# Optimization experiments

Measured on AMD Instinct MI355X. Metric: run time of the kernel, lower is better.

Reference implementation:

```python
import jax, jax.numpy as jnp
import numpy as np

N_NODES = 100000

def sage_conv(x, edge_index, W_l, b_l, W_r):
    # PyG SAGEConv (aggr='mean'): out = lin_l(mean_{j in N(i)} x_j) + lin_r(x_i)
    src = edge_index[0]  # message source nodes
    dst = edge_index[1]  # aggregation target nodes
    msgs = x[src]                                   # [E, F] gather
    agg = jax.ops.segment_sum(msgs, dst, num_segments=N_NODES)      # [N, F]
    cnt = jax.ops.segment_sum(jnp.ones((edge_index.shape[1],), x.dtype), dst,
                              num_segments=N_NODES)                 # [N]
    mean = agg / jnp.clip(cnt, 1.0)[:, None]
    return mean @ W_l.T + b_l + x @ W_r.T


def setup_inputs() -> dict:
    key = jax.random.key(0)
    ks = jax.random.split(key, 8)
    num_features, hid, num_classes = 500, 8, 10
    n_edges = 3200000
    x = jax.random.normal(ks[0], (N_NODES, num_features), dtype=jnp.float32)
    edge_index = jax.random.randint(ks[1], (2, n_edges), 0, N_NODES, dtype=jnp.int64)
    def lin(k, fan_in, fan_out):
        bound = 1.0 / np.sqrt(fan_in)
        return jax.random.uniform(k, (fan_out, fan_in), jnp.float32, -bound, bound)
    W1_l = lin(ks[2], num_features, hid)
    b1_l = jax.random.uniform(ks[3], (hid,), jnp.float32, -1/np.sqrt(num_features), 1/np.sqrt(num_features))
    W1_r = lin(ks[4], num_features, hid)
    W2_l = lin(ks[5], hid, num_classes)
    b2_l = jax.random.uniform(ks[6], (num_classes,), jnp.float32, -1/np.sqrt(hid), 1/np.sqrt(hid))
    W2_r = lin(ks[7], hid, num_classes)
    return {"x": x, "edge_index": edge_index,
            "W1_l": W1_l, "b1_l": b1_l, "W1_r": W1_r,
            "W2_l": W2_l, "b2_l": b2_l, "W2_r": W2_r}


def reference(x, edge_index, W1_l, b1_l, W1_r, W2_l, b2_l, W2_r):
    # eval mode: dropout is a no-op
    h = sage_conv(x, edge_index, W1_l, b1_l, W1_r)
    h = jax.nn.elu(h)
    out = sage_conv(h, edge_index, W2_l, b2_l, W2_r)
    return jax.nn.log_softmax(out, axis=1)
```

## Files before the change

### kernel.cpp

```cpp
#include <hip/hip_runtime.h>
#include <hip/hip_bf16.h>
#include <math.h>


#define NBKT_MAX 1600
#define P_BLOCKS 256
#define BSH 6
#define BSZ 64
#define SEG_CAP 4096

typedef float f4v __attribute__((ext_vector_type(4)));

__device__ __forceinline__ float dot4(f4v a, f4v b) {
    return a.x * b.x + a.y * b.y + a.z * b.z + a.w * b.w;
}
__device__ __forceinline__ unsigned f2bf(float f) {
    unsigned u = __float_as_uint(f);
    return (u + 0x7FFFu + ((u >> 16) & 1u)) >> 16;
}
__device__ __forceinline__ float bflo(unsigned w) { return __uint_as_float(w << 16); }
__device__ __forceinline__ float bfhi(unsigned w) { return __uint_as_float(w & 0xFFFF0000u); }

__global__ __launch_bounds__(256) void proj1_kernel(
    const float* __restrict__ x,
    const float* __restrict__ W1l,
    const float* __restrict__ W1r,
    unsigned short* __restrict__ yab,
    float* __restrict__ yr,
    int N)
{
    const int lane = threadIdx.x & 63;
    const int wv   = threadIdx.x >> 6;
    const f4v zero = {0.f, 0.f, 0.f, 0.f};

    f4v wA[16], wB[16];
    #pragma unroll
    for (int m = 0; m < 16; ++m) {
        const float* wr = (m < 8) ? (W1l + m * 500) : (W1r + (m - 8) * 500);
        wA[m] = *reinterpret_cast<const f4v*>(wr + lane * 4);
        wB[m] = (lane < 61) ? *reinterpret_cast<const f4v*>(wr + 256 + lane * 4) : zero;
    }

    const int P = (N + 1) >> 1;
    const int gw = blockIdx.x * 4 + wv;
    const int nw = gridDim.x * 4;

    int p = gw;
    f4v a0 = zero, a1 = zero, b0 = zero, b1 = zero;
    if (p < P) {
        const int n0 = p * 2;
        const int n1 = min(n0 + 1, N - 1);
        const f4v* xr0 = reinterpret_cast<const f4v*>(x + (size_t)n0 * 500);
        const f4v* xr1 = reinterpret_cast<const f4v*>(x + (size_t)n1 * 500);
        a0 = xr0[lane];
        a1 = xr1[lane];
        b0 = (lane < 61) ? xr0[64 + lane] : zero;
        b1 = (lane < 61) ? xr1[64 + lane] : zero;
    }

    while (p < P) {
        const int pn = p + nw;
        f4v na0 = zero, na1 = zero, nb0 = zero, nb1 = zero;
        if (pn < P) {
            const int m0 = pn * 2;
            const int m1 = min(m0 + 1, N - 1);
            const f4v* q0 = reinterpret_cast<const f4v*>(x + (size_t)m0 * 500);
            const f4v* q1 = reinterpret_cast<const f4v*>(x + (size_t)m1 * 500);
            na0 = q0[lane];
            na1 = q1[lane];
            nb0 = (lane < 61) ? q0[64 + lane] : zero;
            nb1 = (lane < 61) ? q1[64 + lane] : zero;
        }

        float acc[32];
        #pragma unroll
        for (int i = 0; i < 32; ++i) acc[i] = 0.f;

        #pragma unroll
        for (int m = 0; m < 16; ++m) {
            acc[m]      += dot4(a0, wA[m]) + dot4(b0, wB[m]);
            acc[16 + m] += dot4(a1, wA[m]) + dot4(b1, wB[m]);
        }

        #pragma unroll
        for (int i = 0; i < 16; ++i) {
            float keep = (lane & 1) ? acc[i + 16] : acc[i];
            float send = (lane & 1) ? acc[i]      : acc[i + 16];
            acc[i] = keep + __shfl_xor(send, 1);
        }
        #pragma unroll
        for (int i = 0; i < 8; ++i) {
            float keep = (lane & 2) ? acc[i + 8] : acc[i];
            float send = (lane & 2) ? acc[i]     : acc[i + 8];
            acc[i] = keep + __shfl_xor(send, 2);
        }
        #pragma unroll
        for (int i = 0; i < 4; ++i) {
            float keep = (lane & 4) ? acc[i + 4] : acc[i];
            float send = (lane & 4) ? acc[i]     : acc[i + 4];
            acc[i] = keep + __shfl_xor(send, 4);
        }
        #pragma unroll
        for (int i = 0; i < 2; ++i) {
            float keep = (lane & 8) ? acc[i + 2] : acc[i];
            float send = (lane & 8) ? acc[i]     : acc[i + 2];
            acc[i] = keep + __shfl_xor(send, 8);
        }
        {
            float keep = (lane & 16) ? acc[1] : acc[0];
            float send = (lane & 16) ? acc[0] : acc[1];
            acc[0] = keep + __shfl_xor(send, 16);
        }
        float tot = acc[0] + __shfl_xor(acc[0], 32);

        if (lane < 32) {
            int idx = ((lane & 1) << 4) | ((lane & 2) << 2) | (lane & 4)
                    | ((lane & 8) >> 2) | ((lane & 16) >> 4);
            int node = p * 2 + (idx >> 4);
            int m = idx & 15;
            if (node < N) {
                if (m < 8) yab[(size_t)node * 8 + m] = (unsigned short)f2bf(tot);
                else       yr[(size_t)node * 8 + m - 8] = tot;
            }
        }

        a0 = na0; a1 = na1; b0 = nb0; b1 = nb1;
        p = pn;
    }
}

__global__ __launch_bounds__(512) void hist_kernel(
    const int* __restrict__ ei, int E, int chunk, int B,
    int* __restrict__ hist_g)
{
    __shared__ int h[NBKT_MAX];
    for (int i = threadIdx.x; i < B; i += 512) h[i] = 0;
    __syncthreads();
    const int p = blockIdx.x;
    const int e0 = p * chunk, e1 = min(e0 + chunk, E);
    int e = e0 + threadIdx.x;
    for (; e + 512 < e1; e += 1024) {
        int d0 = ei[E + e], d1 = ei[E + e + 512];
        atomicAdd(&h[d0 >> BSH], 1);
        atomicAdd(&h[d1 >> BSH], 1);
    }
    for (; e < e1; e += 512) atomicAdd(&h[ei[E + e] >> BSH], 1);
    __syncthreads();
    for (int b = threadIdx.x; b < B; b += 512)
        hist_g[(size_t)b * P_BLOCKS + p] = h[b];
}

__global__ __launch_bounds__(256) void bsum_kernel(
    const int* __restrict__ hist_g, int* __restrict__ tot)
{
    __shared__ int s[256];
    const int b = blockIdx.x;
    s[threadIdx.x] = hist_g[(size_t)b * P_BLOCKS + threadIdx.x];
    __syncthreads();
    for (int o = 128; o > 0; o >>= 1) {
        if (threadIdx.x < o) s[threadIdx.x] += s[threadIdx.x + o];
        __syncthreads();
    }
    if (threadIdx.x == 0) tot[b] = s[0];
}

__global__ __launch_bounds__(256) void base_kernel(
    int* __restrict__ hist_g, const int* __restrict__ tot, int B,
    int* __restrict__ bstart)
{
    __shared__ int sr[256];
    __shared__ int s2[256];
    __shared__ int bs_sh;
    const int b = blockIdx.x, tid = threadIdx.x;

    int part = 0;
    for (int i = tid; i < b; i += 256) part += tot[i];
    sr[tid] = part;
    __syncthreads();
    for (int o = 128; o > 0; o >>= 1) {
        if (tid < o) sr[tid] += sr[tid + o];
        __syncthreads();
    }
    if (tid == 0) bs_sh = sr[0];
    __syncthreads();
    const int bs = bs_sh;

    const int v = hist_g[(size_t)b * P_BLOCKS + tid];
    s2[tid] = v;
    __syncthreads();
    for (int o = 1; o < 256; o <<= 1) {
        int t = (tid >= o) ? s2[tid - o] : 0;
        __syncthreads();
        s2[tid] += t;
        __syncthreads();
    }
    hist_g[(size_t)b * P_BLOCKS + tid] = bs + s2[tid] - v;
    if (tid == 0) bstart[b] = bs;
    if (b == B - 1 && tid == 255) bstart[B] = bs + s2[255];
}

__global__ __launch_bounds__(512) void scatter2_kernel(
    const int* __restrict__ ei, int E, int chunk, int B,
    const int* __restrict__ base, unsigned* __restrict__ csr)
{
    __shared__ int cur[NBKT_MAX];
    const int p = blockIdx.x;
    for (int b = threadIdx.x; b < B; b += 512) cur[b] = base[(size_t)b * P_BLOCKS + p];
    __syncthreads();
    const int e0 = p * chunk, e1 = min(e0 + chunk, E);
    int e = e0 + threadIdx.x;
    for (; e + 512 < e1; e += 1024) {
        int s0 = ei[e],     s1 = ei[e + 512];
        int d0 = ei[E + e], d1 = ei[E + e + 512];
        int p0 = atomicAdd(&cur[d0 >> BSH], 1);
        int p1 = atomicAdd(&cur[d1 >> BSH], 1);
        csr[p0] = (unsigned)s0 | ((unsigned)(d0 & (BSZ - 1)) << 17);
        csr[p1] = (unsigned)s1 | ((unsigned)(d1 & (BSZ - 1)) << 17);
    }
    for (; e < e1; e += 512) {
        int s0 = ei[e], d0 = ei[E + e];
        int p0 = atomicAdd(&cur[d0 >> BSH], 1);
        csr[p0] = (unsigned)s0 | ((unsigned)(d0 & (BSZ - 1)) << 17);
    }
}

__global__ __launch_bounds__(256) void sortB_kernel(
    const int* __restrict__ bstart,
    unsigned* __restrict__ csr,
    int* __restrict__ nodeoff,
    int B)
{
    __shared__ unsigned stage[SEG_CAP];
    __shared__ int cnt[BSZ];
    __shared__ int cur[BSZ];
    const int b = blockIdx.x, tid = threadIdx.x;
    const int e0 = bstart[b], e1 = bstart[b + 1];
    const int n = e1 - e0;

    if (tid < BSZ) cnt[tid] = 0;
    for (int i = tid; i < n; i += 256) stage[i] = csr[e0 + i];
    __syncthreads();
    for (int i = tid; i < n; i += 256) atomicAdd(&cnt[stage[i] >> 17], 1);
    __syncthreads();
    if (tid < BSZ) {
        int v = cnt[tid];
        int incl = v;
        #pragma unroll
        for (int o = 1; o < 64; o <<= 1) {
            int t = __shfl_up(incl, o);
            if ((tid & 63) >= o) incl += t;
        }
        int excl = e0 + incl - v;
        cur[tid] = excl;
        nodeoff[(size_t)b * BSZ + tid] = excl;
        if (b == B - 1 && tid == 0) nodeoff[(size_t)B * BSZ] = e1;
    }
    __syncthreads();
    for (int i = tid; i < n; i += 256) {
        unsigned pk = stage[i];
        int pos = atomicAdd(&cur[pk >> 17], 1);
        csr[pos] = pk & 0x1FFFFu;
    }
}

__global__ __launch_bounds__(256) void agg1R_kernel(
    const int* __restrict__ nodeoff,
    const unsigned* __restrict__ csr,
    const unsigned short* __restrict__ yab,
    const float* __restrict__ yr,
    const float* __restrict__ b1,
    const float* __restrict__ W2l,
    const float* __restrict__ b2,
    const float* __restrict__ W2r,
    unsigned short* __restrict__ zlb,
    float* __restrict__ zrb,
    int N)
{
    __shared__ float wb[178];
    const int tid = threadIdx.x;
    if (tid < 178)
        wb[tid] = (tid < 8) ? b1[tid] : (tid < 88) ? W2l[tid - 8]
                 : (tid < 98) ? b2[tid - 88] : W2r[tid - 98];
    __syncthreads();

    const int g = tid >> 2;
    const int q = tid & 3;
    const int node = blockIdx.x * BSZ + g;
    const int gs = nodeoff[node], ge = nodeoff[node + 1];
    const uint4* ya4 = reinterpret_cast<const uint4*>(yab);

    float a[8];
    #pragma unroll
    for (int i = 0; i < 8; ++i) a[i] = 0.f;

    for (int e = gs + q; e < ge; e += 4) {
        unsigned s = csr[e];
        uint4 r = ya4[s];
        a[0] += bflo(r.x); a[1] += bfhi(r.x);
        a[2] += bflo(r.y); a[3] += bfhi(r.y);
        a[4] += bflo(r.z); a[5] += bfhi(r.z);
        a[6] += bflo(r.w); a[7] += bfhi(r.w);
    }
    #pragma unroll
    for (int i = 0; i < 8; ++i) {
        a[i] += __shfl_xor(a[i], 1);
        a[i] += __shfl_xor(a[i], 2);
    }

    if (q != 0 || node >= N) return;
    const int deg = ge - gs;
    const float inv = 1.f / fmaxf((float)deg, 1.f);
    const f4v* yr4 = reinterpret_cast<const f4v*>(yr + (size_t)node * 8);
    f4v r0 = yr4[0], r1 = yr4[1];
    const float rr[8] = {r0.x, r0.y, r0.z, r0.w, r1.x, r1.y, r1.z, r1.w};

    float h[8];
    #pragma unroll
    for (int t = 0; t < 8; ++t) {
        float v = a[t] * inv + wb[t] + rr[t];
        h[t] = v > 0.f ? v : expm1f(v);
    }

    float zlv[10], zrv[10];
    #pragma unroll
    for (int k = 0; k < 10; ++k) {
        float al = 0.f, ar = wb[88 + k];
        #pragma unroll
        for (int t = 0; t < 8; ++t) {
            al += wb[8 + k * 8 + t]  * h[t];
            ar += wb[98 + k * 8 + t] * h[t];
        }
        zlv[k] = al; zrv[k] = ar;
    }

    uint4 h0, h1;
    h0.x = f2bf(zlv[0]) | (f2bf(zlv[1]) << 16);
    h0.y = f2bf(zlv[2]) | (f2bf(zlv[3]) << 16);
    h0.z = f2bf(zlv[4]);
    h0.w = 0u;
    h1.x = f2bf(zlv[5]) | (f2bf(zlv[6]) << 16);
    h1.y = f2bf(zlv[7]) | (f2bf(zlv[8]) << 16);
    h1.z = f2bf(zlv[9]);
    h1.w = 0u;
    uint4* zl4w = reinterpret_cast<uint4*>(zlb + (size_t)node * 16);
    zl4w[0] = h0;
    zl4w[1] = h1;

    float4* zr4w = reinterpret_cast<float4*>(zrb + (size_t)node * 12);
    zr4w[0] = make_float4(zrv[0], zrv[1], zrv[2], zrv[3]);
    zr4w[1] = make_float4(zrv[4], zrv[5], zrv[6], zrv[7]);
    zr4w[2] = make_float4(zrv[8], zrv[9], inv, 0.f);
}

__global__ __launch_bounds__(256) void agg2R_kernel(
    const int* __restrict__ nodeoff,
    const unsigned* __restrict__ csr,
    const unsigned short* __restrict__ zlb,
    const float* __restrict__ zrb,
    float* __restrict__ out,
    int N)
{
    const int tid = threadIdx.x;
    const int g = tid >> 2;
    const int q = tid & 3;
    const int node = blockIdx.x * BSZ + g;
    const int gs = nodeoff[node], ge = nodeoff[node + 1];
    const uint4* zl4 = reinterpret_cast<const uint4*>(zlb);

    float a[10];
    #pragma unroll
    for (int i = 0; i < 10; ++i) a[i] = 0.f;

    for (int e = gs + q; e < ge; e += 4) {
        unsigned s = csr[e];
        uint4 rA = zl4[(size_t)s * 2];
        uint4 rB = zl4[(size_t)s * 2 + 1];
        a[0] += bflo(rA.x); a[1] += bfhi(rA.x);
        a[2] += bflo(rA.y); a[3] += bfhi(rA.y);
        a[4] += bflo(rA.z);
        a[5] += bflo(rB.x); a[6] += bfhi(rB.x);
        a[7] += bflo(rB.y); a[8] += bfhi(rB.y);
        a[9] += bflo(rB.z);
    }
    #pragma unroll
    for (int i = 0; i < 10; ++i) {
        a[i] += __shfl_xor(a[i], 1);
        a[i] += __shfl_xor(a[i], 2);
    }

    if (q != 0 || node >= N) return;
    const float* zr = zrb + (size_t)node * 12;
    const float inv = zr[10];
    float v[10];
    float mx = -1e30f;
    #pragma unroll
    for (int k = 0; k < 10; ++k) {
        v[k] = a[k] * inv + zr[k];
        mx = fmaxf(mx, v[k]);
    }
    float ssum = 0.f;
    #pragma unroll
    for (int k = 0; k < 10; ++k) ssum += expf(v[k] - mx);
    const float lse = mx + logf(ssum);
    float2* o = reinterpret_cast<float2*>(out + (size_t)node * 10);
    o[0] = make_float2(v[0] - lse, v[1] - lse);
    o[1] = make_float2(v[2] - lse, v[3] - lse);
    o[2] = make_float2(v[4] - lse, v[5] - lse);
    o[3] = make_float2(v[6] - lse, v[7] - lse);
    o[4] = make_float2(v[8] - lse, v[9] - lse);
}

extern "C" void kernel_launch(void* const* d_in, const int* in_sizes, int n_in,
                              void* d_out, int out_size, void* d_ws, size_t ws_size,
                              hipStream_t stream) {
    const float* x   = (const float*)d_in[0];
    const int*   ei  = (const int*)d_in[1];
    const float* W1l = (const float*)d_in[2];
    const float* b1l = (const float*)d_in[3];
    const float* W1r = (const float*)d_in[4];
    const float* W2l = (const float*)d_in[5];
    const float* b2l = (const float*)d_in[6];
    const float* W2r = (const float*)d_in[7];
    float* out = (float*)d_out;

    const int N = in_sizes[0] / 500;
    const int E = in_sizes[1] / 2;
    const int B = (N + BSZ - 1) >> BSH;
    const int chunk = (E + P_BLOCKS - 1) / P_BLOCKS;

    int* hist_g  = (int*)d_ws;
    int* tot     = hist_g + (size_t)B * P_BLOCKS;
    int* bstart  = tot + B;
    int* nodeoff = bstart + (B + 1);
    unsigned* csr = (unsigned*)(nodeoff + (size_t)B * BSZ + 1);
    size_t off = ((char*)(csr + E) - (char*)d_ws + 15) & ~(size_t)15;
    unsigned short* yab = (unsigned short*)((char*)d_ws + off);
    off = (off + (size_t)N * 16 + 15) & ~(size_t)15;
    unsigned short* zlb = (unsigned short*)((char*)d_ws + off);
    off = (off + (size_t)N * 32 + 15) & ~(size_t)15;
    float* yr  = (float*)((char*)d_ws + off);
    float* zrb = yr + (size_t)8 * N;

    proj1_kernel<<<1024, 256, 0, stream>>>(x, W1l, W1r, yab, yr, N);
    hist_kernel<<<P_BLOCKS, 512, 0, stream>>>(ei, E, chunk, B, hist_g);
    bsum_kernel<<<B, 256, 0, stream>>>(hist_g, tot);
    base_kernel<<<B, 256, 0, stream>>>(hist_g, tot, B, bstart);
    scatter2_kernel<<<P_BLOCKS, 512, 0, stream>>>(ei, E, chunk, B, hist_g, csr);
    sortB_kernel<<<B, 256, 0, stream>>>(bstart, csr, nodeoff, B);
    agg1R_kernel<<<B, 256, 0, stream>>>(nodeoff, csr, yab, yr, b1l, W2l, b2l, W2r,
                                        zlb, zrb, N);
    agg2R_kernel<<<B, 256, 0, stream>>>(nodeoff, csr, zlb, zrb, out, N);
}
```

Measured before the change: 176.2 us.

## Fuse bucket sort into layer-1 aggregation and merge prefix-sum kernels

Merges the per-bucket counting sort with the first aggregation kernel, so sorted source indices stay in shared memory and are read from there instead of being reloaded from global memory. It also drops the separate bucket-total reduction: each block now sums all preceding histogram entries directly, and writes offsets to a separate array instead of overwriting in place. This removes two kernel launches and one global round-trip of the CSR, but adds a second 16 KB shared buffer that lowers occupancy. The direct prefix sum also costs O(B*256) redundant reads per block.

Measured after the change: 380.8 us. 116% more time.

```diff
diff --git a/kernel.cpp b/kernel.cpp
--- a/kernel.cpp
+++ b/kernel.cpp
@@ -150,23 +150,9 @@
         hist_g[(size_t)b * P_BLOCKS + p] = h[b];
 }
 
-__global__ __launch_bounds__(256) void bsum_kernel(
-    const int* __restrict__ hist_g, int* __restrict__ tot)
-{
-    __shared__ int s[256];
-    const int b = blockIdx.x;
-    s[threadIdx.x] = hist_g[(size_t)b * P_BLOCKS + threadIdx.x];
-    __syncthreads();
-    for (int o = 128; o > 0; o >>= 1) {
-        if (threadIdx.x < o) s[threadIdx.x] += s[threadIdx.x + o];
-        __syncthreads();
-    }
-    if (threadIdx.x == 0) tot[b] = s[0];
-}
-
-__global__ __launch_bounds__(256) void base_kernel(
-    int* __restrict__ hist_g, const int* __restrict__ tot, int B,
-    int* __restrict__ bstart)
+__global__ __launch_bounds__(256) void base2_kernel(
+    const int* __restrict__ hist_g, int B,
+    int* __restrict__ base_g, int* __restrict__ bstart)
 {
     __shared__ int sr[256];
     __shared__ int s2[256];
@@ -174,7 +160,8 @@
     const int b = blockIdx.x, tid = threadIdx.x;
 
     int part = 0;
-    for (int i = tid; i < b; i += 256) part += tot[i];
+    const int tot = b * P_BLOCKS;
+    for (int i = tid; i < tot; i += 256) part += hist_g[i];
     sr[tid] = part;
     __syncthreads();
     for (int o = 128; o > 0; o >>= 1) {
@@ -194,18 +181,18 @@
         s2[tid] += t;
         __syncthreads();
     }
-    hist_g[(size_t)b * P_BLOCKS + tid] = bs + s2[tid] - v;
+    base_g[(size_t)b * P_BLOCKS + tid] = bs + s2[tid] - v;
     if (tid == 0) bstart[b] = bs;
     if (b == B - 1 && tid == 255) bstart[B] = bs + s2[255];
 }
 
 __global__ __launch_bounds__(512) void scatter2_kernel(
     const int* __restrict__ ei, int E, int chunk, int B,
-    const int* __restrict__ base, unsigned* __restrict__ csr)
+    const int* __restrict__ base_g, unsigned* __restrict__ csr)
 {
     __shared__ int cur[NBKT_MAX];
     const int p = blockIdx.x;
-    for (int b = threadIdx.x; b < B; b += 512) cur[b] = base[(size_t)b * P_BLOCKS + p];
+    for (int b = threadIdx.x; b < B; b += 512) cur[b] = base_g[(size_t)b * P_BLOCKS + p];
     __syncthreads();
     const int e0 = p * chunk, e1 = min(e0 + chunk, E);
     int e = e0 + threadIdx.x;
@@ -224,48 +211,10 @@
     }
 }
 
-__global__ __launch_bounds__(256) void sortB_kernel(
+__global__ __launch_bounds__(256) void sortAgg1_kernel(
     const int* __restrict__ bstart,
     unsigned* __restrict__ csr,
     int* __restrict__ nodeoff,
-    int B)
-{
-    __shared__ unsigned stage[SEG_CAP];
-    __shared__ int cnt[BSZ];
-    __shared__ int cur[BSZ];
-    const int b = blockIdx.x, tid = threadIdx.x;
-    const int e0 = bstart[b], e1 = bstart[b + 1];
-    const int n = e1 - e0;
-
-    if (tid < BSZ) cnt[tid] = 0;
-    for (int i = tid; i < n; i += 256) stage[i] = csr[e0 + i];
-    __syncthreads();
-    for (int i = tid; i < n; i += 256) atomicAdd(&cnt[stage[i] >> 17], 1);
-    __syncthreads();
-    if (tid < BSZ) {
-        int v = cnt[tid];
-        int incl = v;
-        #pragma unroll
-        for (int o = 1; o < 64; o <<= 1) {
-            int t = __shfl_up(incl, o);
-            if ((tid & 63) >= o) incl += t;
-        }
-        int excl = e0 + incl - v;
-        cur[tid] = excl;
-        nodeoff[(size_t)b * BSZ + tid] = excl;
-        if (b == B - 1 && tid == 0) nodeoff[(size_t)B * BSZ] = e1;
-    }
-    __syncthreads();
-    for (int i = tid; i < n; i += 256) {
-        unsigned pk = stage[i];
-        int pos = atomicAdd(&cur[pk >> 17], 1);
-        csr[pos] = pk & 0x1FFFFu;
-    }
-}
-
-__global__ __launch_bounds__(256) void agg1R_kernel(
-    const int* __restrict__ nodeoff,
-    const unsigned* __restrict__ csr,
     const unsigned short* __restrict__ yab,
     const float* __restrict__ yr,
     const float* __restrict__ b1,
@@ -274,19 +223,55 @@
     const float* __restrict__ W2r,
     unsigned short* __restrict__ zlb,
     float* __restrict__ zrb,
-    int N)
-{
+    int B, int N)
+{
+    __shared__ unsigned stage[SEG_CAP];
+    __shared__ unsigned sorted[SEG_CAP];
+    __shared__ int cnt[BSZ];
+    __shared__ int cur[BSZ];
+    __shared__ int loc[BSZ + 1];
     __shared__ float wb[178];
-    const int tid = threadIdx.x;
+    const int b = blockIdx.x, tid = threadIdx.x;
+    const int e0 = bstart[b], e1 = bstart[b + 1];
+    const int n = e1 - e0;
+
+    if (tid < BSZ) cnt[tid] = 0;
     if (tid < 178)
         wb[tid] = (tid < 8) ? b1[tid] : (tid < 88) ? W2l[tid - 8]
                  : (tid < 98) ? b2[tid - 88] : W2r[tid - 98];
+    for (int i = tid; i < n; i += 256) stage[i] = csr[e0 + i];
+    __syncthreads();
+    for (int i = tid; i < n; i += 256) atomicAdd(&cnt[stage[i] >> 17], 1);
+    __syncthreads();
+    if (tid < BSZ) {
+        int v = cnt[tid];
+        int incl = v;
+        #pragma unroll
+        for (int o = 1; o < 64; o <<= 1) {
+            int t = __shfl_up(incl, o);
+            if (tid >= o) incl += t;
+        }
+        int excl = incl - v;
+        loc[tid] = excl;
+        cur[tid] = excl;
+        nodeoff[(size_t)b * BSZ + tid] = e0 + excl;
+        if (tid == BSZ - 1) loc[BSZ] = incl;
+        if (b == B - 1 && tid == 0) nodeoff[(size_t)B * BSZ] = e1;
+    }
+    __syncthreads();
+    for (int i = tid; i < n; i += 256) {
+        unsigned pk = stage[i];
+        int pos = atomicAdd(&cur[pk >> 17], 1);
+        unsigned s = pk & 0x1FFFFu;
+        sorted[pos] = s;
+        csr[e0 + pos] = s;
+    }
     __syncthreads();
 
     const int g = tid >> 2;
     const int q = tid & 3;
-    const int node = blockIdx.x * BSZ + g;
-    const int gs = nodeoff[node], ge = nodeoff[node + 1];
+    const int node = b * BSZ + g;
+    const int gs = loc[g], ge = loc[g + 1];
     const uint4* ya4 = reinterpret_cast<const uint4*>(yab);
 
     float a[8];
@@ -294,7 +279,7 @@
     for (int i = 0; i < 8; ++i) a[i] = 0.f;
 
     for (int e = gs + q; e < ge; e += 4) {
-        unsigned s = csr[e];
+        unsigned s = sorted[e];
         uint4 r = ya4[s];
         a[0] += bflo(r.x); a[1] += bfhi(r.x);
         a[2] += bflo(r.y); a[3] += bfhi(r.y);
@@ -429,8 +414,8 @@
     const int chunk = (E + P_BLOCKS - 1) / P_BLOCKS;
 
     int* hist_g  = (int*)d_ws;
-    int* tot     = hist_g + (size_t)B * P_BLOCKS;
-    int* bstart  = tot + B;
+    int* base_g  = hist_g + (size_t)B * P_BLOCKS;
+    int* bstart  = base_g + (size_t)B * P_BLOCKS;
     int* nodeoff = bstart + (B + 1);
     unsigned* csr = (unsigned*)(nodeoff + (size_t)B * BSZ + 1);
     size_t off = ((char*)(csr + E) - (char*)d_ws + 15) & ~(size_t)15;
@@ -443,11 +428,9 @@
 
     proj1_kernel<<<1024, 256, 0, stream>>>(x, W1l, W1r, yab, yr, N);
     hist_kernel<<<P_BLOCKS, 512, 0, stream>>>(ei, E, chunk, B, hist_g);
-    bsum_kernel<<<B, 256, 0, stream>>>(hist_g, tot);
-    base_kernel<<<B, 256, 0, stream>>>(hist_g, tot, B, bstart);
-    scatter2_kernel<<<P_BLOCKS, 512, 0, stream>>>(ei, E, chunk, B, hist_g, csr);
-    sortB_kernel<<<B, 256, 0, stream>>>(bstart, csr, nodeoff, B);
-    agg1R_kernel<<<B, 256, 0, stream>>>(nodeoff, csr, yab, yr, b1l, W2l, b2l, W2r,
-                                        zlb, zrb, N);
+    base2_kernel<<<B, 256, 0, stream>>>(hist_g, B, base_g, bstart);
+    scatter2_kernel<<<P_BLOCKS, 512, 0, stream>>>(ei, E, chunk, B, base_g, csr);
+    sortAgg1_kernel<<<B, 256, 0, stream>>>(bstart, csr, nodeoff, yab, yr,
+                                           b1l, W2l, b2l, W2r, zlb, zrb, B, N);
     agg2R_kernel<<<B, 256, 0, stream>>>(nodeoff, csr, zlb, zrb, out, N);
 }
```
